# Performance work log

Hardware: AMD Instinct MI355X
Metric: run time of the kernel (lower is better)

The kernel has to match this reference:

```python
import jax, jax.numpy as jnp
import numpy as np

B, S, D, H = 16, 512, 768, 12
DH = D // H  # 64


def sparsemax(z):
    # sparsemax along last axis (Martins & Astudillo 2016); shift-invariant
    z = z - jax.lax.stop_gradient(jnp.max(z, axis=-1, keepdims=True))
    z_sorted = -jnp.sort(-z, axis=-1)                      # descending
    K = z.shape[-1]
    k = jnp.arange(1, K + 1, dtype=z.dtype)                # [K]
    z_cum = jnp.cumsum(z_sorted, axis=-1)
    support = (1.0 + k * z_sorted) > z_cum                 # [..., K] bool
    k_z = jnp.sum(support, axis=-1, keepdims=True).astype(z.dtype)
    # tau = (sum of supported entries - 1) / k_z
    z_cum_k = jnp.take_along_axis(z_cum, jnp.sum(support, axis=-1, keepdims=True) - 1, axis=-1)
    tau = (z_cum_k - 1.0) / k_z
    return jnp.maximum(z - tau, 0.0)


def setup_inputs() -> dict:
    key = jax.random.key(0)
    ks = jax.random.split(key, 4)
    scale = 1.0 / np.sqrt(D)
    return {
        "hidden_states": jax.random.normal(ks[0], (B, S, D), jnp.float32),
        "attention_mask": jnp.zeros((B, 1, 1, S), jnp.float32),
        "Wq": jax.random.normal(ks[1], (D, D), jnp.float32) * scale,
        "bq": jnp.zeros((D,), jnp.float32),
        "Wk": jax.random.normal(ks[2], (D, D), jnp.float32) * scale,
        "bk": jnp.zeros((D,), jnp.float32),
        "Wv": jax.random.normal(ks[3], (D, D), jnp.float32) * scale,
        "bv": jnp.zeros((D,), jnp.float32),
    }


def reference(hidden_states, attention_mask, Wq, bq, Wk, bk, Wv, bv):
    def heads(x):  # [B,S,D] -> [B,H,S,DH]
        return x.reshape(B, S, H, DH).transpose(0, 2, 1, 3)

    q = heads(hidden_states @ Wq.T + bq)
    k = heads(hidden_states @ Wk.T + bk)
    v = heads(hidden_states @ Wv.T + bv)

    scores = jnp.einsum("bhqd,bhkd->bhqk", q, k) / np.sqrt(DH).astype(np.float32)
    scores = scores + attention_mask                       # additive mask broadcast
    probs = sparsemax(scores)                              # [B,H,S,S]
    ctx = jnp.einsum("bhqk,bhkd->bhqd", probs, v)          # [B,H,S,DH]
    return ctx.transpose(0, 2, 1, 3).reshape(B, S, D)
```

## Files before the change

kernel.cpp:

```cpp
#include <hip/hip_runtime.h>
#include <math.h>

#define B_ 16
#define S_ 512
#define D_ 768
#define H_ 12
#define DH_ 64
#define BH_ (B_*H_)
#define MTOT (B_*S_)
#define NTOT (3*D_)

typedef unsigned short ushort_t;
typedef __attribute__((ext_vector_type(8))) _Float16 f16x8;
typedef __attribute__((ext_vector_type(4))) float f32x4;

__device__ __forceinline__ ushort_t f2h(float x){
    union { _Float16 h; ushort_t u; } c;
    c.h = (_Float16)x;
    return c.u;
}

__device__ __forceinline__ void cp16(const void* g, void* l){
    __builtin_amdgcn_global_load_lds(
        (const __attribute__((address_space(1))) unsigned int*)g,
        (__attribute__((address_space(3))) unsigned int*)l, 16, 0, 0);
}

__global__ __launch_bounds__(256)
void convert_x(const float* __restrict__ src, ushort_t* __restrict__ dst, int n4)
{
    int i = blockIdx.x * 256 + threadIdx.x;
    if (i >= n4) return;
    float4 x = ((const float4*)src)[i];
    union { ushort_t u[4]; uint2 v; } p;
    p.u[0] = f2h(x.x); p.u[1] = f2h(x.y);
    p.u[2] = f2h(x.z); p.u[3] = f2h(x.w);
    ((uint2*)dst)[i] = p.v;
}

__global__ __launch_bounds__(256)
void convert_w(const float* __restrict__ Wq, const float* __restrict__ Wk,
               const float* __restrict__ Wv, ushort_t* __restrict__ dst)
{
    const float* src = (blockIdx.z==0) ? Wq : (blockIdx.z==1) ? Wk : Wv;
    const int n4 = D_*D_/4;
    int i = blockIdx.x * 256 + threadIdx.x;
    if (i >= n4) return;
    size_t off4 = (size_t)blockIdx.z * n4;
    float4 x = ((const float4*)src)[i];
    union { ushort_t u[4]; uint2 v; } p;
    p.u[0] = f2h(x.x); p.u[1] = f2h(x.y);
    p.u[2] = f2h(x.z); p.u[3] = f2h(x.w);
    ((uint2*)dst)[off4 + i] = p.v;
}

#define BM 128
#define BN 128
#define BK 32

__global__ __launch_bounds__(256)
void gemm_f16(const ushort_t* __restrict__ A, const ushort_t* __restrict__ Bw,
              const float* __restrict__ bq, const float* __restrict__ bk,
              const float* __restrict__ bv,
              ushort_t* __restrict__ qf, ushort_t* __restrict__ kf,
              float* __restrict__ outv)
{
    __shared__ ushort_t Ah[BM*BK], Bh[BN*BK];

    const int tid  = threadIdx.x;
    const int lane = tid & 63, wave = tid >> 6;

    const int n = blockIdx.y * 18 + blockIdx.x;
    const int nn = (n & 7) * 144 + (n >> 3);
    const int bx = nn % 18, by = nn / 18;
    const int m0 = by * BM, n0 = bx * BN;
    const int wm = (wave >> 1) * 64, wn = (wave & 1) * 64;

    f32x4 acc[4][4];
    #pragma unroll
    for (int i=0;i<4;i++)
        #pragma unroll
        for (int j=0;j<4;j++) acc[i][j] = (f32x4){0.f,0.f,0.f,0.f};

    const int r0 = tid >> 2, c0 = (tid & 3) * 8;
    const size_t ga0 = (size_t)(m0 + r0)      * D_ + c0;
    const size_t ga1 = (size_t)(m0 + 64 + r0) * D_ + c0;
    const size_t gb0 = (size_t)(n0 + r0)      * D_ + c0;
    const size_t gb1 = (size_t)(n0 + 64 + r0) * D_ + c0;
    const int l0 = wave * 512;
    const int l1 = 2048 + wave * 512;

    const int fr = lane & 15, kc = (lane >> 4) * 8;

    for (int k0 = 0; k0 < D_; k0 += BK) {
        cp16(A  + ga0 + k0, Ah + l0);
        cp16(A  + ga1 + k0, Ah + l1);
        cp16(Bw + gb0 + k0, Bh + l0);
        cp16(Bw + gb1 + k0, Bh + l1);
        __syncthreads();

        f16x8 fa[4], fb[4];
        #pragma unroll
        for (int i = 0; i < 4; i++){
            fa[i] = *(const f16x8*)&Ah[(wm + i*16 + fr)*BK + kc];
            fb[i] = *(const f16x8*)&Bh[(wn + i*16 + fr)*BK + kc];
        }
        #pragma unroll
        for (int i = 0; i < 4; i++)
            #pragma unroll
            for (int j = 0; j < 4; j++)
                acc[i][j] = __builtin_amdgcn_mfma_f32_16x16x32_f16(fa[i], fb[j], acc[i][j], 0,0,0);
        __syncthreads();
    }

    const int mat = n0 / D_;
    const float* bias = (mat==0) ? bq : (mat==1) ? bk : bv;
    const int col = lane & 15, rbase = (lane >> 4) * 4;
    #pragma unroll
    for (int j = 0; j < 4; j++){
        int nc = n0 + wn + j*16 + col - mat*D_;
        int h = nc >> 6, d = nc & 63;
        float bsv = bias[nc];
        #pragma unroll
        for (int i = 0; i < 4; i++){
            #pragma unroll
            for (int r = 0; r < 4; r++){
                int m = m0 + wm + i*16 + rbase + r;
                int bb = m >> 9, s = m & 511;
                size_t idx = (((size_t)bb*H_ + h)*S_ + s)*DH_ + d;
                float val = acc[i][j][r] + bsv;
                if (mat == 2) outv[idx] = val;
                else if (mat == 0) qf[idx] = f2h(val);
                else               kf[idx] = f2h(val);
            }
        }
    }
}

#define SROW 320

__global__ __launch_bounds__(256)
void attn_mfma(const ushort_t* __restrict__ Qf, const ushort_t* __restrict__ Kf,
               const float* __restrict__ V, const float* __restrict__ mask,
               float* __restrict__ out)
{
    __shared__ float sc[16*SROW];

    const int lane = threadIdx.x & 63;
    const int wave = threadIdx.x >> 6;
    const int fr = lane & 15, quad = lane >> 4;

    const int orig = blockIdx.x;
    const int swz  = (orig & 7) * (BH_*32/8) + (orig >> 3);
    const int bh = swz >> 5;
    const int q0 = (swz & 31) * 16;
    const int b = bh / H_, h = bh % H_;
    const size_t hb = (size_t)bh * S_ * DH_;

    f16x8 qh[2];
    {
        const ushort_t* qp = Qf + hb + (size_t)(q0 + fr)*DH_ + quad*8;
        qh[0] = *(const f16x8*)qp;
        qh[1] = *(const f16x8*)(qp + 32);
    }

    f32x4 acc2[2][4];
    #pragma unroll
    for (int h2=0;h2<2;h2++)
        #pragma unroll
        for (int jj=0;jj<4;jj++) acc2[h2][jj] = (f32x4){0.f,0.f,0.f,0.f};

    __builtin_amdgcn_s_setprio(1);
    #pragma unroll
    for (int h2=0;h2<2;h2++){
        #pragma unroll
        for (int jj=0;jj<4;jj++){
            int kt = h2*256 + wave*64 + jj*16;
            const ushort_t* kp = Kf + hb + (size_t)(kt + fr)*DH_ + quad*8;
            f16x8 k0 = *(const f16x8*)kp;
            f16x8 k1 = *(const f16x8*)(kp + 32);
            f32x4 a = acc2[h2][jj];
            a = __builtin_amdgcn_mfma_f32_16x16x32_f16(qh[0], k0, a, 0,0,0);
            a = __builtin_amdgcn_mfma_f32_16x16x32_f16(qh[1], k1, a, 0,0,0);
            acc2[h2][jj] = a;
        }
    }
    __builtin_amdgcn_s_setprio(0);

    const float* mrow = mask + b * S_;
    const int row = wave*4 + quad;
    float z[32];

    #pragma unroll
    for (int jj=0;jj<4;jj++){
        int k = wave*64 + jj*16 + fr;
        float mv = mrow[k];
        int o = wave*4 + jj;
        #pragma unroll
        for (int r=0;r<4;r++)
            sc[(quad*4+r)*SROW + o*20 + fr] = acc2[0][jj][r]*0.125f + mv;
    }
    __syncthreads();
    {
        const float* zp = &sc[row*SROW + fr*20];
        #pragma unroll
        for (int jj=0;jj<4;jj++){
            float4 t = *(const float4*)(zp + jj*4);
            z[jj*4+0]=t.x; z[jj*4+1]=t.y; z[jj*4+2]=t.z; z[jj*4+3]=t.w;
        }
    }
    __syncthreads();
    #pragma unroll
    for (int jj=0;jj<4;jj++){
        int k = 256 + wave*64 + jj*16 + fr;
        float mv = mrow[k];
        int o = wave*4 + jj;
        #pragma unroll
        for (int r=0;r<4;r++)
            sc[(quad*4+r)*SROW + o*20 + fr] = acc2[1][jj][r]*0.125f + mv;
    }
    __syncthreads();
    {
        const float* zp = &sc[row*SROW + fr*20];
        #pragma unroll
        for (int jj=0;jj<4;jj++){
            float4 t = *(const float4*)(zp + jj*4);
            z[16+jj*4+0]=t.x; z[16+jj*4+1]=t.y; z[16+jj*4+2]=t.z; z[16+jj*4+3]=t.w;
        }
    }

    float tau;
    {
        float red[16];
        #pragma unroll
        for (int i=0;i<16;i++) red[i] = fmaxf(z[i], z[i+16]);
        #pragma unroll
        for (int i=0;i<8;i++)  red[i] = fmaxf(red[i], red[i+8]);
        #pragma unroll
        for (int i=0;i<4;i++)  red[i] = fmaxf(red[i], red[i+4]);
        float mm = fmaxf(fmaxf(red[0],red[1]), fmaxf(red[2],red[3]));
        #pragma unroll
        for (int off=1; off<16; off<<=1) mm = fmaxf(mm, __shfl_xor(mm, off, 64));
        tau = mm - 1.0f;
    }

    for (int it=0; it<16; it++){
        float s0=0.f,s1=0.f,s2=0.f,s3=0.f;
        float k0=0.f,k1=0.f,k2=0.f,k3=0.f;
        #pragma unroll
        for (int i=0;i<32;i+=4){
            float z0=z[i], z1=z[i+1], z2=z[i+2], z3=z[i+3];
            if (z0 > tau){ s0 += z0; k0 += 1.f; }
            if (z1 > tau){ s1 += z1; k1 += 1.f; }
            if (z2 > tau){ s2 += z2; k2 += 1.f; }
            if (z3 > tau){ s3 += z3; k3 += 1.f; }
        }
        float ss = (s0+s1)+(s2+s3), kk = (k0+k1)+(k2+k3);
        #pragma unroll
        for (int off=1; off<16; off<<=1){
            ss += __shfl_xor(ss, off, 64);
            kk += __shfl_xor(kk, off, 64);
        }
        float tn = (ss - 1.0f) / kk;
        bool changed = (tn != tau);
        tau = tn;
        if (!__any(changed)) break;
    }

    float4 ctx = make_float4(0.f, 0.f, 0.f, 0.f);
    const float* vb = V + hb;
    #pragma unroll
    for (int i=0;i<32;i++){
        float p = z[i] - tau;
        unsigned long long bal = __ballot(p > 0.f);
        unsigned mk = (unsigned)((bal >> (quad*16)) & 0xFFFFull);
        const int base_i = (i < 16) ? i : (240 + i);
        while (mk){
            int s = __ffs(mk) - 1;
            mk &= mk - 1;
            float pv = __shfl(p, quad*16 + s, 64);
            const float4 vv = *(const float4*)(vb + (size_t)(base_i + s*16)*DH_ + fr*4);
            ctx.x += pv * vv.x;
            ctx.y += pv * vv.y;
            ctx.z += pv * vv.z;
            ctx.w += pv * vv.w;
        }
    }

    *(float4*)(out + (size_t)(b*S_ + q0 + row)*D_ + h*DH_ + fr*4) = ctx;
}

extern "C" void kernel_launch(void* const* d_in, const int* in_sizes, int n_in,
                              void* d_out, int out_size, void* d_ws, size_t ws_size,
                              hipStream_t stream) {
    const float* hs   = (const float*)d_in[0];
    const float* mask = (const float*)d_in[1];
    const float* Wq   = (const float*)d_in[2];
    const float* bq   = (const float*)d_in[3];
    const float* Wk   = (const float*)d_in[4];
    const float* bk   = (const float*)d_in[5];
    const float* Wv   = (const float*)d_in[6];
    const float* bv   = (const float*)d_in[7];
    float* out = (float*)d_out;

    const size_t per = (size_t)BH_ * S_ * DH_;
    char* w = (char*)d_ws;
    float*    vb  = (float*)w;    w += per*4;
    ushort_t* qf  = (ushort_t*)w; w += per*2;
    ushort_t* kf  = (ushort_t*)w; w += per*2;
    ushort_t* Xf  = (ushort_t*)w; w += per*2;
    ushort_t* Wf  = (ushort_t*)w;

    convert_x<<<(int)(per/4/256), 256, 0, stream>>>(hs, Xf, (int)(per/4));
    convert_w<<<dim3(D_*D_/4/256, 1, 3), 256, 0, stream>>>(Wq, Wk, Wv, Wf);

    dim3 ggrid(NTOT/BN, MTOT/BM);
    gemm_f16<<<ggrid, 256, 0, stream>>>(Xf, Wf, bq, bk, bv, qf, kf, vb);

    attn_mfma<<<BH_*32, 256, 0, stream>>>(qf, kf, vb, mask, out);
}
```

Before: 230.0 us.

## Compact sparsemax candidates into shared-memory lists for tau iteration and PV

After the row max is known, each row's scores above max-1 are compacted into a shared-memory list of values and key indices, using an atomic counter per row and a cap of 64. When no row overflows the cap, the tau fixed-point iteration runs over at most 4 values per lane instead of 32, and the PV accumulation walks the compact list with 4 independent V loads at a time. This replaces the ballot/ffs/shuffle loop. The change adds a block sync, shared atomics and a fallback path that is kept for rows that overflow. It may also add divergence and extra LDS traffic.

```diff
diff --git a/kernel.cpp b/kernel.cpp
--- a/kernel.cpp
+++ b/kernel.cpp
@@ -138,6 +138,7 @@
 }
 
 #define SROW 320
+#define LCAP 64
 
 __global__ __launch_bounds__(256)
 void attn_mfma(const ushort_t* __restrict__ Qf, const ushort_t* __restrict__ Kf,
@@ -145,10 +146,13 @@
                float* __restrict__ out)
 {
     __shared__ float sc[16*SROW];
+    __shared__ int Lcnt[16];
 
     const int lane = threadIdx.x & 63;
     const int wave = threadIdx.x >> 6;
     const int fr = lane & 15, quad = lane >> 4;
+
+    if (threadIdx.x < 16) Lcnt[threadIdx.x] = 0;
 
     const int orig = blockIdx.x;
     const int swz  = (orig & 7) * (BH_*32/8) + (orig >> 3);
@@ -228,8 +232,9 @@
             z[16+jj*4+0]=t.x; z[16+jj*4+1]=t.y; z[16+jj*4+2]=t.z; z[16+jj*4+3]=t.w;
         }
     }
-
-    float tau;
+    __syncthreads();
+
+    float mm;
     {
         float red[16];
         #pragma unroll
@@ -238,52 +243,120 @@
         for (int i=0;i<8;i++)  red[i] = fmaxf(red[i], red[i+8]);
         #pragma unroll
         for (int i=0;i<4;i++)  red[i] = fmaxf(red[i], red[i+4]);
-        float mm = fmaxf(fmaxf(red[0],red[1]), fmaxf(red[2],red[3]));
+        mm = fmaxf(fmaxf(red[0],red[1]), fmaxf(red[2],red[3]));
         #pragma unroll
         for (int off=1; off<16; off<<=1) mm = fmaxf(mm, __shfl_xor(mm, off, 64));
-        tau = mm - 1.0f;
-    }
-
-    for (int it=0; it<16; it++){
-        float s0=0.f,s1=0.f,s2=0.f,s3=0.f;
-        float k0=0.f,k1=0.f,k2=0.f,k3=0.f;
-        #pragma unroll
-        for (int i=0;i<32;i+=4){
-            float z0=z[i], z1=z[i+1], z2=z[i+2], z3=z[i+3];
-            if (z0 > tau){ s0 += z0; k0 += 1.f; }
-            if (z1 > tau){ s1 += z1; k1 += 1.f; }
-            if (z2 > tau){ s2 += z2; k2 += 1.f; }
-            if (z3 > tau){ s3 += z3; k3 += 1.f; }
-        }
-        float ss = (s0+s1)+(s2+s3), kk = (k0+k1)+(k2+k3);
-        #pragma unroll
-        for (int off=1; off<16; off<<=1){
-            ss += __shfl_xor(ss, off, 64);
-            kk += __shfl_xor(kk, off, 64);
-        }
-        float tn = (ss - 1.0f) / kk;
-        bool changed = (tn != tau);
-        tau = tn;
-        if (!__any(changed)) break;
+    }
+    const float tau0 = mm - 1.0f;
+    float tau = tau0;
+
+    float* Lval = sc;
+    int*   Lkey = (int*)(sc + 16*LCAP);
+    {
+        int c = 0;
+        #pragma unroll
+        for (int i=0;i<32;i++) c += (z[i] > tau0) ? 1 : 0;
+        int o = atomicAdd(&Lcnt[row], c);
+        #pragma unroll
+        for (int i=0;i<32;i++){
+            if (z[i] > tau0){
+                if (o < LCAP){
+                    Lval[row*LCAP + o] = z[i];
+                    Lkey[row*LCAP + o] = fr*16 + ((i<16) ? i : (240 + i));
+                }
+                o++;
+            }
+        }
+    }
+    const int cnt = Lcnt[row];
+    const bool fast = !__any(cnt > LCAP);
+
+    if (fast){
+        float v0 = (fr      < cnt) ? Lval[row*LCAP + fr     ] : -1e30f;
+        float v1 = (fr + 16 < cnt) ? Lval[row*LCAP + fr + 16] : -1e30f;
+        float v2 = (fr + 32 < cnt) ? Lval[row*LCAP + fr + 32] : -1e30f;
+        float v3 = (fr + 48 < cnt) ? Lval[row*LCAP + fr + 48] : -1e30f;
+        for (int it=0; it<16; it++){
+            float ss=0.f, kk=0.f;
+            if (v0 > tau){ ss+=v0; kk+=1.f; }
+            if (v1 > tau){ ss+=v1; kk+=1.f; }
+            if (v2 > tau){ ss+=v2; kk+=1.f; }
+            if (v3 > tau){ ss+=v3; kk+=1.f; }
+            #pragma unroll
+            for (int off=1; off<16; off<<=1){
+                ss += __shfl_xor(ss, off, 64);
+                kk += __shfl_xor(kk, off, 64);
+            }
+            float tn = (ss - 1.0f) / kk;
+            bool changed = (tn != tau);
+            tau = tn;
+            if (!__any(changed)) break;
+        }
+    } else {
+        for (int it=0; it<16; it++){
+            float s0=0.f,s1=0.f,s2=0.f,s3=0.f;
+            float k0=0.f,k1=0.f,k2=0.f,k3=0.f;
+            #pragma unroll
+            for (int i=0;i<32;i+=4){
+                float z0=z[i], z1=z[i+1], z2=z[i+2], z3=z[i+3];
+                if (z0 > tau){ s0 += z0; k0 += 1.f; }
+                if (z1 > tau){ s1 += z1; k1 += 1.f; }
+                if (z2 > tau){ s2 += z2; k2 += 1.f; }
+                if (z3 > tau){ s3 += z3; k3 += 1.f; }
+            }
+            float ss = (s0+s1)+(s2+s3), kk = (k0+k1)+(k2+k3);
+            #pragma unroll
+            for (int off=1; off<16; off<<=1){
+                ss += __shfl_xor(ss, off, 64);
+                kk += __shfl_xor(kk, off, 64);
+            }
+            float tn = (ss - 1.0f) / kk;
+            bool changed = (tn != tau);
+            tau = tn;
+            if (!__any(changed)) break;
+        }
     }
 
     float4 ctx = make_float4(0.f, 0.f, 0.f, 0.f);
     const float* vb = V + hb;
-    #pragma unroll
-    for (int i=0;i<32;i++){
-        float p = z[i] - tau;
-        unsigned long long bal = __ballot(p > 0.f);
-        unsigned mk = (unsigned)((bal >> (quad*16)) & 0xFFFFull);
-        const int base_i = (i < 16) ? i : (240 + i);
-        while (mk){
-            int s = __ffs(mk) - 1;
-            mk &= mk - 1;
-            float pv = __shfl(p, quad*16 + s, 64);
-            const float4 vv = *(const float4*)(vb + (size_t)(base_i + s*16)*DH_ + fr*4);
-            ctx.x += pv * vv.x;
-            ctx.y += pv * vv.y;
-            ctx.z += pv * vv.z;
-            ctx.w += pv * vv.w;
+    if (fast){
+        for (int j0 = 0; j0 < cnt; j0 += 4){
+            float p[4]; float4 vv[4];
+            #pragma unroll
+            for (int u=0; u<4; ++u){
+                int j = j0 + u;
+                bool in = j < cnt;
+                float val = in ? Lval[row*LCAP + j] : 0.f;
+                int   key = in ? Lkey[row*LCAP + j] : 0;
+                float pp = val - tau;
+                p[u] = (in && pp > 0.f) ? pp : 0.f;
+                vv[u] = *(const float4*)(vb + (size_t)key*DH_ + fr*4);
+            }
+            #pragma unroll
+            for (int u=0; u<4; ++u){
+                ctx.x += p[u]*vv[u].x;
+                ctx.y += p[u]*vv[u].y;
+                ctx.z += p[u]*vv[u].z;
+                ctx.w += p[u]*vv[u].w;
+            }
+        }
+    } else {
+        #pragma unroll
+        for (int i=0;i<32;i++){
+            float p = z[i] - tau;
+            unsigned long long bal = __ballot(p > 0.f);
+            unsigned mk = (unsigned)((bal >> (quad*16)) & 0xFFFFull);
+            const int base_i = (i < 16) ? i : (240 + i);
+            while (mk){
+                int s = __ffs(mk) - 1;
+                mk &= mk - 1;
+                float pv = __shfl(p, quad*16 + s, 64);
+                const float4 vv = *(const float4*)(vb + (size_t)(base_i + s*16)*DH_ + fr*4);
+                ctx.x += pv * vv.x;
+                ctx.y += pv * vv.y;
+                ctx.z += pv * vv.z;
+                ctx.w += pv * vv.w;
+            }
         }
     }
 
```

Measured after the change: 232.3 us. Within noise of the previous version (+1.0%).
